# Optimization experiments

Measured on AMD Instinct MI355X. Metric: run time of the kernel, lower is better.

Reference implementation:

```python
import jax, jax.numpy as jnp
import numpy as np

N_NODES = 50000
N_EDGES = 800000
IN_DIM = 128
EDGE_DIM = 16
N_HEADS = 8
OUT_DIM = 16  # per head


def setup_inputs() -> dict:
    key = jax.random.key(0)
    ks = jax.random.split(key, 6)
    x = jax.random.normal(ks[0], (N_NODES, IN_DIM), dtype=jnp.float32)
    edge_attr = jax.random.normal(ks[1], (N_EDGES, EDGE_DIM), dtype=jnp.float32)
    W_node = jax.random.normal(ks[2], (N_HEADS, IN_DIM, OUT_DIM), dtype=jnp.float32) * 0.1
    W_edge = jax.random.normal(ks[3], (N_HEADS, EDGE_DIM, OUT_DIM), dtype=jnp.float32) * 0.1
    src = jax.random.randint(ks[4], (N_EDGES,), 0, N_NODES, dtype=jnp.int32)
    dst = jax.random.randint(ks[5], (N_EDGES,), 0, N_NODES, dtype=jnp.int32)
    return {"x": x, "edge_attr": edge_attr, "W_node": W_node, "W_edge": W_edge,
            "src": src, "dst": dst}


def reference(x, edge_attr, W_node, W_edge, src, dst):
    # Multi-head edge-gated GAT layer (EG_GATLayer), use_edge=use_gate=True.
    H, _, D = W_node.shape
    N = x.shape[0]
    scale = 1.0 / jnp.sqrt(jnp.asarray(D, x.dtype))

    h = jnp.einsum('ni,hid->nhd', x, W_node)          # [N,H,D] per-head node proj
    e = jnp.einsum('ei,hid->ehd', edge_attr, W_edge)  # [E,H,D] per-head edge proj

    q = h[dst]                                        # [E,H,D] gather dst nodes
    k = h[src]                                        # [E,H,D] gather src nodes

    # edge-conditioned attention logits, LeakyReLU as in GAT
    logits = ((q * k).sum(-1) + e.sum(-1)) * scale    # [E,H]
    logits = jax.nn.leaky_relu(logits, 0.2)

    # segment softmax over each destination node's incoming edges
    m = jax.ops.segment_max(logits, dst, num_segments=N)  # [N,H]
    m = jnp.where(jnp.isfinite(m), m, 0.0)
    m = jax.lax.stop_gradient(m)
    ex = jnp.exp(logits - m[dst])                     # [E,H]
    denom = jax.ops.segment_sum(ex, dst, num_segments=N)  # [N,H]
    alpha = ex / (denom[dst] + 1e-9)                  # [E,H]

    # edge-gated messages, scatter-aggregate to dst
    msg = k * jax.nn.sigmoid(e) * alpha[..., None]    # [E,H,D]
    out = jax.ops.segment_sum(msg, dst, num_segments=N)   # [N,H,D]
    return out.reshape(N, H * D)                      # concat heads
```

## Files before the change

### kernel.cpp

```cpp
#include <hip/hip_runtime.h>
#include <math.h>


#define LOG2E 1.44269504088896340736f
#define C_QK  0.36067376022224085f

typedef _Float16 h2 __attribute__((ext_vector_type(2)));
typedef _Float16 h4 __attribute__((ext_vector_type(4)));
typedef _Float16 h8 __attribute__((ext_vector_type(8)));
typedef float    f4 __attribute__((ext_vector_type(4)));

__device__ __forceinline__ float fdot2(h2 a, h2 b, float c) {
    return __builtin_amdgcn_fdot2(a, b, c, false);
}
__device__ __forceinline__ h2 bch(unsigned u) {
    return __builtin_bit_cast(h2, u);
}
__device__ __forceinline__ unsigned pkh2(float a, float b) {
    h2 p = { (_Float16)a, (_Float16)b };
    return __builtin_bit_cast(unsigned, p);
}

#define DPP_ADD(x, ctrl)                                                       \
    x += __builtin_bit_cast(float, __builtin_amdgcn_update_dpp(                \
             0, __builtin_bit_cast(int, x), (ctrl), 0xF, 0xF, false))

__global__ __launch_bounds__(256) void k_gemm(
    const float* __restrict__ x, const float* __restrict__ Wn,
    _Float16* __restrict__ h16, int N)
{
    int lane = threadIdx.x & 63, wid = threadIdx.x >> 6;
    int rt = blockIdx.x * 4 + wid;
    if (rt * 16 >= N) return;
    int r = lane & 15, kb = lane >> 4;

    const float* xrow = x + (size_t)(rt * 16 + r) * 128 + kb * 8;
    h8 A[4];
#pragma unroll
    for (int kk = 0; kk < 4; ++kk) {
        f4 a0 = *(const f4*)(xrow + kk * 32);
        f4 a1 = *(const f4*)(xrow + kk * 32 + 4);
        A[kk] = h8{(_Float16)a0.x,(_Float16)a0.y,(_Float16)a0.z,(_Float16)a0.w,
                   (_Float16)a1.x,(_Float16)a1.y,(_Float16)a1.z,(_Float16)a1.w};
    }

    for (int h = 0; h < 8; ++h) {
        const float* wb = Wn + h * 2048 + (kb * 8) * 16 + r;
        f4 acc = {0.f, 0.f, 0.f, 0.f};
#pragma unroll
        for (int kk = 0; kk < 4; ++kk) {
            const float* wk = wb + (size_t)kk * 32 * 16;
            h8 B;
#pragma unroll
            for (int i = 0; i < 8; ++i) B[i] = (_Float16)wk[i * 16];
            acc = __builtin_amdgcn_mfma_f32_16x16x32_f16(A[kk], B, acc, 0, 0, 0);
        }
#pragma unroll
        for (int j = 0; j < 4; ++j) {
            h16[(size_t)(rt * 16 + 4 * kb + j) * 128 + h * 16 + r] =
                (_Float16)acc[j];
        }
    }
}

__global__ __launch_bounds__(256) void k_prep(
    const float* __restrict__ ea, const float* __restrict__ We,
    const int* __restrict__ src, const int* __restrict__ dst,
    _Float16* __restrict__ ea16, int2* __restrict__ csrbin,
    int* __restrict__ counts, unsigned* __restrict__ gatetab, int E)
{
    int t = threadIdx.x;
    int e = blockIdx.x * 256 + t;
    if (e < E) {
        int dn = dst[e];
        int r = atomicAdd(counts + dn, 1);
        csrbin[((size_t)dn << 6) + r] = make_int2(e << 5, src[e] << 8);
        const float4* ap = (const float4*)(ea + (size_t)e * 16);
        float4 a0 = ap[0], a1 = ap[1], a2 = ap[2], a3 = ap[3];
        h4* op = (h4*)(ea16 + ((size_t)e << 4));
        op[0] = h4{(_Float16)a0.x, (_Float16)a0.y, (_Float16)a0.z, (_Float16)a0.w};
        op[1] = h4{(_Float16)a1.x, (_Float16)a1.y, (_Float16)a1.z, (_Float16)a1.w};
        op[2] = h4{(_Float16)a2.x, (_Float16)a2.y, (_Float16)a2.z, (_Float16)a2.w};
        op[3] = h4{(_Float16)a3.x, (_Float16)a3.y, (_Float16)a3.z, (_Float16)a3.w};
    }

    if (blockIdx.x == gridDim.x - 1 && t < 64) {
        int lane = t;
        int head = lane >> 3, dd = lane & 7, d0 = dd * 2;
        const float* Wh = We + head * 256;
        unsigned* row = gatetab + lane * 20;
#pragma unroll
        for (int i = 0; i < 8; ++i) {
            row[i]     = pkh2(Wh[(2*i)*16 + d0]     * -LOG2E,
                              Wh[(2*i+1)*16 + d0]   * -LOG2E);
            row[8 + i] = pkh2(Wh[(2*i)*16 + d0 + 1] * -LOG2E,
                              Wh[(2*i+1)*16 + d0+1] * -LOG2E);
        }
        float cs0 = 0.f, cs1 = 0.f;
#pragma unroll
        for (int k = 0; k < 16; ++k) {
            cs0 += Wh[d0 * 16 + k];
            cs1 += Wh[(d0 + 1) * 16 + k];
        }
        row[16] = pkh2(cs0, cs1);
    }
}

__global__ __launch_bounds__(256) void k_alloc(
    const int* __restrict__ counts, int2* __restrict__ seg,
    int* __restrict__ gcur, int N)
{
    int i = blockIdx.x * 256 + threadIdx.x;
    int lane = threadIdx.x & 63;
    int v = (i < N) ? counts[i] : 0;
    int incl = v;
#pragma unroll
    for (int o = 1; o < 64; o <<= 1) {
        int u = __shfl_up(incl, o);
        if (lane >= o) incl += u;
    }
    int total = __shfl(incl, 63);
    int base = 0;
    if (lane == 63) base = atomicAdd(gcur, total);
    base = __shfl(base, 63);
    int st = base + incl - v;
    if (i < N) seg[i] = make_int2(st, v);
}

__global__ __launch_bounds__(256) void k_compact(
    const int2* __restrict__ csrbin, const int2* __restrict__ seg,
    int2* __restrict__ csr, int N)
{
    int t = threadIdx.x;
    int lane = t & 63, wid = t >> 6;
    int n = blockIdx.x * 4 + wid;
    if (n >= N) return;
    int2 sg = seg[n];
    if (lane < sg.y)
        csr[sg.x + lane] = csrbin[((size_t)n << 6) + lane];
}

__global__ __launch_bounds__(64) void k_fused11(
    const _Float16* __restrict__ h16, const _Float16* __restrict__ ea16,
    const int2* __restrict__ csr, const unsigned* __restrict__ gatetab,
    const int2* __restrict__ seg, float* __restrict__ out, int N)
{
    int lane = threadIdx.x;
    int n = blockIdx.x;
    int dd = lane & 7;

    const uint4* tb = (const uint4*)(gatetab + lane * 20);
    uint4 t0 = tb[0], t1 = tb[1], t2 = tb[2], t3 = tb[3];
    h2 cs2 = bch(gatetab[lane * 20 + 16]);
    h2 wa[8], wb[8];
    wa[0]=bch(t0.x); wa[1]=bch(t0.y); wa[2]=bch(t0.z); wa[3]=bch(t0.w);
    wa[4]=bch(t1.x); wa[5]=bch(t1.y); wa[6]=bch(t1.z); wa[7]=bch(t1.w);
    wb[0]=bch(t2.x); wb[1]=bch(t2.y); wb[2]=bch(t2.z); wb[3]=bch(t2.w);
    wb[4]=bch(t3.x); wb[5]=bch(t3.y); wb[6]=bch(t3.z); wb[7]=bch(t3.w);

    const char* hb = (const char*)h16;
    const char* eb = (const char*)ea16;
    unsigned l4 = (unsigned)lane << 2;
    unsigned dd4 = (unsigned)dd << 2;

    h2 q2 = *(const h2*)(hb + ((size_t)n << 8) + l4);
    int2 sg = seg[n];
    int s0  = __builtin_amdgcn_readfirstlane(sg.x);
    int deg = __builtin_amdgcn_readfirstlane(sg.y);

    float acc0 = 0.f, acc1 = 0.f, den = 0.f;
#pragma unroll 4
    for (int j = 0; j < deg; ++j) {
        int2 ce = csr[s0 + j];
        unsigned eoff = (unsigned)ce.x;
        h2 kv2 = *(const h2*)(hb + (unsigned)ce.y + l4);
        uint4 r0 = *(const uint4*)(eb + eoff);
        uint4 r1 = *(const uint4*)(eb + eoff + 16);
        h2 ea2 = *(const h2*)(eb + eoff + dd4);

        float part = fdot2(q2, kv2, 0.f);
        part = fdot2(ea2, cs2, part);
        DPP_ADD(part, 0xB1);
        DPP_ADD(part, 0x4E);
        DPP_ADD(part, 0x141);

        float y  = part * C_QK;
        float lg = fmaxf(y, 0.2f * y);
        float pa = exp2f(lg);

        float ev0 = 0.f, ev1 = 0.f;
        ev0 = fdot2(bch(r0.x), wa[0], ev0);  ev1 = fdot2(bch(r0.x), wb[0], ev1);
        ev0 = fdot2(bch(r0.y), wa[1], ev0);  ev1 = fdot2(bch(r0.y), wb[1], ev1);
        ev0 = fdot2(bch(r0.z), wa[2], ev0);  ev1 = fdot2(bch(r0.z), wb[2], ev1);
        ev0 = fdot2(bch(r0.w), wa[3], ev0);  ev1 = fdot2(bch(r0.w), wb[3], ev1);
        ev0 = fdot2(bch(r1.x), wa[4], ev0);  ev1 = fdot2(bch(r1.x), wb[4], ev1);
        ev0 = fdot2(bch(r1.y), wa[5], ev0);  ev1 = fdot2(bch(r1.y), wb[5], ev1);
        ev0 = fdot2(bch(r1.z), wa[6], ev0);  ev1 = fdot2(bch(r1.z), wb[6], ev1);
        ev0 = fdot2(bch(r1.w), wa[7], ev0);  ev1 = fdot2(bch(r1.w), wb[7], ev1);
        float sg0 = __builtin_amdgcn_rcpf(1.f + exp2f(ev0));
        float sg1 = __builtin_amdgcn_rcpf(1.f + exp2f(ev1));

        den += pa;
        acc0 = fmaf(pa * sg0, (float)kv2.x, acc0);
        acc1 = fmaf(pa * sg1, (float)kv2.y, acc1);
    }
    float idn = __builtin_amdgcn_rcpf(den + 1e-9f);
    *(float2*)(out + ((size_t)n << 7) + (lane << 1)) =
        make_float2(acc0 * idn, acc1 * idn);
}

extern "C" void kernel_launch(void* const* d_in, const int* in_sizes, int n_in,
                              void* d_out, int out_size, void* d_ws, size_t ws_size,
                              hipStream_t stream)
{
    const float* x  = (const float*)d_in[0];
    const float* ea = (const float*)d_in[1];
    const float* Wn = (const float*)d_in[2];
    const float* We = (const float*)d_in[3];
    const int*  src = (const int*)d_in[4];
    const int*  dst = (const int*)d_in[5];
    float* out = (float*)d_out;

    int N = in_sizes[0] / 128;
    int E = in_sizes[4];

    char* ws = (char*)d_ws;
    int2*      csrbin = (int2*)ws;
    int2*      csr    = (int2*)(ws + (size_t)N * 512);
    _Float16*  ea16   = (_Float16*)(ws + (size_t)N * 512 + (size_t)E * 8);
    _Float16*  h16    = ea16 + (size_t)E * 16;
    int2*      seg    = (int2*)(h16 + (size_t)N * 128);
    int*       counts = (int*)(seg + N);
    int*       gcur   = counts + N;
    unsigned*  gatetab= (unsigned*)(gcur + 1);

    hipMemsetAsync(counts, 0, (size_t)(N + 1) * sizeof(int), stream);

    int nRT = (N + 15) / 16;
    k_gemm   <<<(nRT + 3) / 4,   256, 0, stream>>>(x, Wn, h16, N);
    k_prep   <<<(E + 255) / 256, 256, 0, stream>>>(ea, We, src, dst, ea16,
                                                   csrbin, counts, gatetab, E);
    k_alloc  <<<(N + 255) / 256, 256, 0, stream>>>(counts, seg, gcur, N);
    k_compact<<<(N + 3) / 4,     256, 0, stream>>>(csrbin, seg, csr, N);
    k_fused11<<<N,               64, 0, stream>>>(h16, ea16, csr, gatetab,
                                                  seg, out, N);
}
```

Measured before the change: 182.0 us.

## Merge GEMM with edge prep and fuse alloc with compaction kernel

Combines the node projection GEMM and edge preprocessing into one launch by splitting the grid into edge blocks and GEMM blocks. It also merges the segment allocation scan and CSR compaction into one kernel, where each wavefront loops over its 64 nodes and copies their bins. This cuts two kernel launches and lets the independent GEMM and edge work overlap. The fused compaction runs a serial 64-iteration loop per wave with fewer threads than the old one-wave-per-node layout, so it may expose less parallelism.

```diff
diff --git a/kernel.cpp b/kernel.cpp
--- a/kernel.cpp
+++ b/kernel.cpp
@@ -25,12 +25,55 @@
     x += __builtin_bit_cast(float, __builtin_amdgcn_update_dpp(                \
              0, __builtin_bit_cast(int, x), (ctrl), 0xF, 0xF, false))
 
-__global__ __launch_bounds__(256) void k_gemm(
+__global__ __launch_bounds__(256) void k_eg(
     const float* __restrict__ x, const float* __restrict__ Wn,
-    _Float16* __restrict__ h16, int N)
-{
-    int lane = threadIdx.x & 63, wid = threadIdx.x >> 6;
-    int rt = blockIdx.x * 4 + wid;
+    const float* __restrict__ ea, const float* __restrict__ We,
+    const int* __restrict__ src, const int* __restrict__ dst,
+    _Float16* __restrict__ h16, _Float16* __restrict__ ea16,
+    int2* __restrict__ csrbin, int* __restrict__ counts,
+    unsigned* __restrict__ gatetab, int N, int E, int nEdgeB)
+{
+    int t = threadIdx.x;
+
+    if ((int)blockIdx.x < nEdgeB) {
+        int e = blockIdx.x * 256 + t;
+        if (e < E) {
+            int dn = dst[e];
+            int r = atomicAdd(counts + dn, 1);
+            csrbin[((size_t)dn << 6) + r] = make_int2(e << 5, src[e] << 8);
+            const float4* ap = (const float4*)(ea + (size_t)e * 16);
+            float4 a0 = ap[0], a1 = ap[1], a2 = ap[2], a3 = ap[3];
+            h4* op = (h4*)(ea16 + ((size_t)e << 4));
+            op[0] = h4{(_Float16)a0.x, (_Float16)a0.y, (_Float16)a0.z, (_Float16)a0.w};
+            op[1] = h4{(_Float16)a1.x, (_Float16)a1.y, (_Float16)a1.z, (_Float16)a1.w};
+            op[2] = h4{(_Float16)a2.x, (_Float16)a2.y, (_Float16)a2.z, (_Float16)a2.w};
+            op[3] = h4{(_Float16)a3.x, (_Float16)a3.y, (_Float16)a3.z, (_Float16)a3.w};
+        }
+        if ((int)blockIdx.x == nEdgeB - 1 && t < 64) {
+            int lane = t;
+            int head = lane >> 3, dd = lane & 7, d0 = dd * 2;
+            const float* Wh = We + head * 256;
+            unsigned* row = gatetab + lane * 20;
+#pragma unroll
+            for (int i = 0; i < 8; ++i) {
+                row[i]     = pkh2(Wh[(2*i)*16 + d0]     * -LOG2E,
+                                  Wh[(2*i+1)*16 + d0]   * -LOG2E);
+                row[8 + i] = pkh2(Wh[(2*i)*16 + d0 + 1] * -LOG2E,
+                                  Wh[(2*i+1)*16 + d0+1] * -LOG2E);
+            }
+            float cs0 = 0.f, cs1 = 0.f;
+#pragma unroll
+            for (int k = 0; k < 16; ++k) {
+                cs0 += Wh[d0 * 16 + k];
+                cs1 += Wh[(d0 + 1) * 16 + k];
+            }
+            row[16] = pkh2(cs0, cs1);
+        }
+        return;
+    }
+
+    int lane = t & 63, wid = t >> 6;
+    int rt = ((int)blockIdx.x - nEdgeB) * 4 + wid;
     if (rt * 16 >= N) return;
     int r = lane & 15, kb = lane >> 4;
 
@@ -63,51 +106,9 @@
     }
 }
 
-__global__ __launch_bounds__(256) void k_prep(
-    const float* __restrict__ ea, const float* __restrict__ We,
-    const int* __restrict__ src, const int* __restrict__ dst,
-    _Float16* __restrict__ ea16, int2* __restrict__ csrbin,
-    int* __restrict__ counts, unsigned* __restrict__ gatetab, int E)
-{
-    int t = threadIdx.x;
-    int e = blockIdx.x * 256 + t;
-    if (e < E) {
-        int dn = dst[e];
-        int r = atomicAdd(counts + dn, 1);
-        csrbin[((size_t)dn << 6) + r] = make_int2(e << 5, src[e] << 8);
-        const float4* ap = (const float4*)(ea + (size_t)e * 16);
-        float4 a0 = ap[0], a1 = ap[1], a2 = ap[2], a3 = ap[3];
-        h4* op = (h4*)(ea16 + ((size_t)e << 4));
-        op[0] = h4{(_Float16)a0.x, (_Float16)a0.y, (_Float16)a0.z, (_Float16)a0.w};
-        op[1] = h4{(_Float16)a1.x, (_Float16)a1.y, (_Float16)a1.z, (_Float16)a1.w};
-        op[2] = h4{(_Float16)a2.x, (_Float16)a2.y, (_Float16)a2.z, (_Float16)a2.w};
-        op[3] = h4{(_Float16)a3.x, (_Float16)a3.y, (_Float16)a3.z, (_Float16)a3.w};
-    }
-
-    if (blockIdx.x == gridDim.x - 1 && t < 64) {
-        int lane = t;
-        int head = lane >> 3, dd = lane & 7, d0 = dd * 2;
-        const float* Wh = We + head * 256;
-        unsigned* row = gatetab + lane * 20;
-#pragma unroll
-        for (int i = 0; i < 8; ++i) {
-            row[i]     = pkh2(Wh[(2*i)*16 + d0]     * -LOG2E,
-                              Wh[(2*i+1)*16 + d0]   * -LOG2E);
-            row[8 + i] = pkh2(Wh[(2*i)*16 + d0 + 1] * -LOG2E,
-                              Wh[(2*i+1)*16 + d0+1] * -LOG2E);
-        }
-        float cs0 = 0.f, cs1 = 0.f;
-#pragma unroll
-        for (int k = 0; k < 16; ++k) {
-            cs0 += Wh[d0 * 16 + k];
-            cs1 += Wh[(d0 + 1) * 16 + k];
-        }
-        row[16] = pkh2(cs0, cs1);
-    }
-}
-
-__global__ __launch_bounds__(256) void k_alloc(
-    const int* __restrict__ counts, int2* __restrict__ seg,
+__global__ __launch_bounds__(256) void k_allocpact(
+    const int* __restrict__ counts, const int2* __restrict__ csrbin,
+    int2* __restrict__ csr, int2* __restrict__ seg,
     int* __restrict__ gcur, int N)
 {
     int i = blockIdx.x * 256 + threadIdx.x;
@@ -125,19 +126,15 @@
     base = __shfl(base, 63);
     int st = base + incl - v;
     if (i < N) seg[i] = make_int2(st, v);
-}
-
-__global__ __launch_bounds__(256) void k_compact(
-    const int2* __restrict__ csrbin, const int2* __restrict__ seg,
-    int2* __restrict__ csr, int N)
-{
-    int t = threadIdx.x;
-    int lane = t & 63, wid = t >> 6;
-    int n = blockIdx.x * 4 + wid;
-    if (n >= N) return;
-    int2 sg = seg[n];
-    if (lane < sg.y)
-        csr[sg.x + lane] = csrbin[((size_t)n << 6) + lane];
+
+    int nbase = blockIdx.x * 256 + (threadIdx.x & ~63);
+    for (int k = 0; k < 64; ++k) {
+        int stk = __shfl(st, k);
+        int dk  = __shfl(v, k);
+        int nk  = nbase + k;
+        if (lane < dk)
+            csr[stk + lane] = csrbin[((size_t)nk << 6) + lane];
+    }
 }
 
 __global__ __launch_bounds__(64) void k_fused11(
@@ -236,12 +233,13 @@
 
     hipMemsetAsync(counts, 0, (size_t)(N + 1) * sizeof(int), stream);
 
-    int nRT = (N + 15) / 16;
-    k_gemm   <<<(nRT + 3) / 4,   256, 0, stream>>>(x, Wn, h16, N);
-    k_prep   <<<(E + 255) / 256, 256, 0, stream>>>(ea, We, src, dst, ea16,
-                                                   csrbin, counts, gatetab, E);
-    k_alloc  <<<(N + 255) / 256, 256, 0, stream>>>(counts, seg, gcur, N);
-    k_compact<<<(N + 3) / 4,     256, 0, stream>>>(csrbin, seg, csr, N);
-    k_fused11<<<N,               64, 0, stream>>>(h16, ea16, csr, gatetab,
-                                                  seg, out, N);
-}
+    int nEdgeB = (E + 255) / 256;
+    int nGemmB = ((N + 15) / 16 + 3) / 4;
+    k_eg       <<<nEdgeB + nGemmB, 256, 0, stream>>>(x, Wn, ea, We, src, dst,
+                                                     h16, ea16, csrbin, counts,
+                                                     gatetab, N, E, nEdgeB);
+    k_allocpact<<<(N + 255) / 256, 256, 0, stream>>>(counts, csrbin, csr, seg,
+                                                     gcur, N);
+    k_fused11  <<<N,               64, 0, stream>>>(h16, ea16, csr, gatetab,
+                                                    seg, out, N);
+}
```

Measured after the change: 190.4 us. 4.6% more time.
